# Kernel tuning notes

Measured on AMD Instinct MI355X. Metric: run time of the kernel, lower is better.

## Reference

```python
import jax, jax.numpy as jnp
import numpy as np

B, N, DIM, HEADS, RED = 8, 1024, 768, 12, 2
CR = DIM // RED  # 384 reduced channel dim
HD = CR // HEADS  # 32 head dim
EPS = 1e-5


def layer_norm(x, g, b):
    mu = jnp.mean(x, axis=-1, keepdims=True)
    var = jnp.var(x, axis=-1, keepdims=True)
    return (x - mu) * jax.lax.rsqrt(var + EPS) * g + b


def setup_inputs() -> dict:
    key = jax.random.key(0)
    ks = jax.random.split(key, 8)
    s_in = 1.0 / np.sqrt(DIM)
    s_cr = 1.0 / np.sqrt(CR)
    return {
        "x": jax.random.normal(ks[0], (B, N, DIM), dtype=jnp.float32),
        "ln0_g": jnp.ones((DIM,), jnp.float32),
        "ln0_b": jnp.zeros((DIM,), jnp.float32),
        "w_proj": jax.random.normal(ks[1], (CR, DIM), jnp.float32) * s_in,  # conv1x1 -> linear
        "b_proj": jnp.zeros((CR,), jnp.float32),
        "ln1_g": jnp.ones((CR,), jnp.float32),
        "ln1_b": jnp.zeros((CR,), jnp.float32),
        "wq": jax.random.normal(ks[2], (CR, CR), jnp.float32) * s_cr,
        "wk": jax.random.normal(ks[3], (CR, CR), jnp.float32) * s_cr,
        "wv": jax.random.normal(ks[4], (CR, CR), jnp.float32) * s_cr,
    }


def attention(y, wq, wk, wv):
    # y: [B, N, CR]; 1x1 conv == linear on channel dim
    def heads(w):
        return (y @ w.T).reshape(B, N, HEADS, HD).transpose(0, 2, 1, 3)  # [B,H,N,D]
    q, k, v = heads(wq), heads(wk), heads(wv)
    scale = HD ** -0.5
    attn = jax.nn.softmax(jnp.einsum("bhnd,bhmd->bhnm", q, k) * scale, axis=-1)
    out = jnp.einsum("bhnm,bhmd->bhnd", attn, v)  # [B,H,N,D]
    return out.transpose(0, 2, 1, 3).reshape(B, N, CR)


def reference(x, ln0_g, ln0_b, w_proj, b_proj, ln1_g, ln1_b, wq, wk, wv):
    h = layer_norm(x, ln0_g, ln0_b) @ w_proj.T + b_proj  # [B,N,CR]
    y = layer_norm(h, ln1_g, ln1_b)
    return h + attention(y, wq, wk, wv)
```

## Files before the change

### kernel.cpp

```cpp
#include <hip/hip_runtime.h>
#include <hip/hip_bf16.h>
#include <math.h>

#define BB 8
#define NN 1024
#define DIM 768
#define HEADS 12
#define CR 384
#define HD 32
#define MROWS (BB*NN)
#define EPS 1e-5f
#define SCALE_Q 0.25503486f

typedef __attribute__((ext_vector_type(8))) __bf16 bf16x8;
typedef __attribute__((ext_vector_type(8))) unsigned short u16x8;
typedef __attribute__((ext_vector_type(4))) float f32x4;

__device__ __forceinline__ unsigned short f2bf(float f) {
    unsigned int u = __float_as_uint(f);
    u += 0x7fffu + ((u >> 16) & 1u);
    return (unsigned short)(u >> 16);
}

__device__ __forceinline__ unsigned int packbf2(float lo, float hi) {
    __hip_bfloat162 h2 = __float22bfloat162_rn(make_float2(lo, hi));
    unsigned int u; __builtin_memcpy(&u, &h2, sizeof(u));
    return u;
}

__device__ __forceinline__ void async_cp16(const unsigned short* g, unsigned short* l) {
    __builtin_amdgcn_global_load_lds(
        (const __attribute__((address_space(1))) unsigned int*)g,
        (__attribute__((address_space(3))) unsigned int*)l, 16, 0, 0);
}

__global__ __launch_bounds__(256) void ln0_cast(
    const float* __restrict__ x,
    const float* __restrict__ g, const float* __restrict__ bt,
    unsigned short* __restrict__ a0,
    const float* __restrict__ wpf, const float* __restrict__ wq,
    const float* __restrict__ wk, const float* __restrict__ wv,
    unsigned short* __restrict__ wpo, unsigned short* __restrict__ wqkvo)
{
    const int bx = blockIdx.x;
    const int t = threadIdx.x;
    if (bx >= MROWS) {
        int i = (bx - MROWS) * 256 + t;
        const float* src; unsigned short* dst; int off;
        if (i < 73728) { src = wpf; dst = wpo; off = i; }
        else {
            int j = i - 73728;
            int sel = j / 36864; off = j % 36864;
            src = sel == 0 ? wq : (sel == 1 ? wk : wv);
            dst = wqkvo + (size_t)sel * 147456;
        }
        float4 v = ((const float4*)src)[off];
        ((ushort4*)dst)[off] = make_ushort4(f2bf(v.x), f2bf(v.y), f2bf(v.z), f2bf(v.w));
        return;
    }
    const int nv = DIM >> 2;
    const float* a = x + (size_t)bx * DIM;
    float4 val = make_float4(0.f, 0.f, 0.f, 0.f);
    float s = 0.f, ss = 0.f;
    if (t < nv) {
        val = ((const float4*)a)[t];
        s = val.x + val.y + val.z + val.w;
        ss = val.x * val.x + val.y * val.y + val.z * val.z + val.w * val.w;
    }
    for (int off = 32; off; off >>= 1) {
        s  += __shfl_down(s, off, 64);
        ss += __shfl_down(ss, off, 64);
    }
    __shared__ float rS[4], rSS[4];
    __shared__ float sh_mu, sh_rs;
    int lane = t & 63, w = t >> 6;
    if (lane == 0) { rS[w] = s; rSS[w] = ss; }
    __syncthreads();
    if (t == 0) {
        float S = rS[0] + rS[1] + rS[2] + rS[3];
        float SS = rSS[0] + rSS[1] + rSS[2] + rSS[3];
        float m = S / DIM;
        sh_mu = m;
        sh_rs = rsqrtf(SS / DIM - m * m + EPS);
    }
    __syncthreads();
    if (t < nv) {
        float m = sh_mu, r = sh_rs;
        float4 gv = ((const float4*)g)[t];
        float4 bv = ((const float4*)bt)[t];
        ((ushort4*)(a0 + (size_t)bx * DIM))[t] = make_ushort4(
            f2bf((val.x - m) * r * gv.x + bv.x),
            f2bf((val.y - m) * r * gv.y + bv.y),
            f2bf((val.z - m) * r * gv.z + bv.z),
            f2bf((val.w - m) * r * gv.w + bv.w));
    }
}

__global__ __launch_bounds__(128) void ln1_sum(
    const float* __restrict__ h0, const float* __restrict__ h1,
    const float* __restrict__ bias,
    const float* __restrict__ g, const float* __restrict__ bt,
    float* __restrict__ hs, unsigned short* __restrict__ y)
{
    const int row = blockIdx.x;
    const int t = threadIdx.x;
    const int nv = CR >> 2;
    float4 val = make_float4(0.f, 0.f, 0.f, 0.f);
    float s = 0.f, ss = 0.f;
    if (t < nv) {
        float4 v0 = ((const float4*)(h0 + (size_t)row * CR))[t];
        float4 v1 = ((const float4*)(h1 + (size_t)row * CR))[t];
        float4 bv = ((const float4*)bias)[t];
        val = make_float4(v0.x + v1.x + bv.x, v0.y + v1.y + bv.y,
                          v0.z + v1.z + bv.z, v0.w + v1.w + bv.w);
        ((float4*)(hs + (size_t)row * CR))[t] = val;
        s = val.x + val.y + val.z + val.w;
        ss = val.x * val.x + val.y * val.y + val.z * val.z + val.w * val.w;
    }
    for (int off = 32; off; off >>= 1) {
        s  += __shfl_down(s, off, 64);
        ss += __shfl_down(ss, off, 64);
    }
    __shared__ float rS[2], rSS[2];
    __shared__ float sh_mu, sh_rs;
    int lane = t & 63, w = t >> 6;
    if (lane == 0) { rS[w] = s; rSS[w] = ss; }
    __syncthreads();
    if (t == 0) {
        float S = rS[0] + rS[1];
        float SS = rSS[0] + rSS[1];
        float m = S / CR;
        sh_mu = m;
        sh_rs = rsqrtf(SS / CR - m * m + EPS);
    }
    __syncthreads();
    if (t < nv) {
        float m = sh_mu, r = sh_rs;
        float4 gv = ((const float4*)g)[t];
        float4 bv = ((const float4*)bt)[t];
        ((ushort4*)(y + (size_t)row * CR))[t] = make_ushort4(
            f2bf((val.x - m) * r * gv.x + bv.x),
            f2bf((val.y - m) * r * gv.y + bv.y),
            f2bf((val.z - m) * r * gv.z + bv.z),
            f2bf((val.w - m) * r * gv.w + bv.w));
    }
}

template<int KD, int NITER, int MODE>
__global__ __launch_bounds__(256) void gemm_mfma(
    const unsigned short* __restrict__ A,
    const unsigned short* __restrict__ W,
    void* __restrict__ C0, void* __restrict__ C1)
{
    __shared__ unsigned short Asm[2 * 128 * 32];
    __shared__ unsigned short Bsm[2 * 128 * 32];
    const int t = threadIdx.x;
    const int wave = t >> 6, lane = t & 63;
    const int l15 = lane & 15, quad = lane >> 4;
    const int m0 = blockIdx.y * 128;
    const int n0 = blockIdx.x * 128;
    const int koff = blockIdx.z * (NITER * 32);
    const int wm = (wave & 1) * 64, wn = (wave >> 1) * 64;

    const int srow = lane >> 2;
    const int skq  = (lane & 3) * 8;
    const unsigned short* gA = A + (size_t)(m0 + wave * 32 + srow) * KD + koff + skq;
    const unsigned short* gB = W + (size_t)(n0 + wave * 32 + srow) * KD + koff + skq;
    unsigned short* lA = Asm + wave * 1024;
    unsigned short* lB = Bsm + wave * 1024;

    async_cp16(gA, lA);
    async_cp16(gA + (size_t)16 * KD, lA + 512);
    async_cp16(gB, lB);
    async_cp16(gB + (size_t)16 * KD, lB + 512);

    f32x4 acc[4][4];
#pragma unroll
    for (int i = 0; i < 4; i++)
#pragma unroll
        for (int j = 0; j < 4; j++) acc[i][j] = (f32x4){0.f, 0.f, 0.f, 0.f};

    for (int it = 0; it < NITER; it++) {
        __syncthreads();
        const int cur = it & 1;
        if (it + 1 < NITER) {
            const int noff = (cur ^ 1) * 4096;
            async_cp16(gA + (it + 1) * 32, lA + noff);
            async_cp16(gA + (size_t)16 * KD + (it + 1) * 32, lA + noff + 512);
            async_cp16(gB + (it + 1) * 32, lB + noff);
            async_cp16(gB + (size_t)16 * KD + (it + 1) * 32, lB + noff + 512);
        }
        const unsigned short* Ab = Asm + cur * 4096;
        const unsigned short* Bb = Bsm + cur * 4096;
        bf16x8 af[4], bfr[4];
#pragma unroll
        for (int i = 0; i < 4; i++)
            af[i] = *(const bf16x8*)(Ab + (wm + i * 16 + l15) * 32 + quad * 8);
#pragma unroll
        for (int j = 0; j < 4; j++)
            bfr[j] = *(const bf16x8*)(Bb + (wn + j * 16 + l15) * 32 + quad * 8);
#pragma unroll
        for (int i = 0; i < 4; i++)
#pragma unroll
            for (int j = 0; j < 4; j++)
                acc[i][j] = __builtin_amdgcn_mfma_f32_16x16x32_bf16(af[i], bfr[j], acc[i][j], 0, 0, 0);
    }

    if constexpr (MODE == 0) {
        float* C = (float*)C0 + (size_t)blockIdx.z * MROWS * CR;
#pragma unroll
        for (int i = 0; i < 4; i++)
#pragma unroll
            for (int j = 0; j < 4; j++)
#pragma unroll
                for (int reg = 0; reg < 4; reg++) {
                    int row = m0 + wm + i * 16 + quad * 4 + reg;
                    int col = n0 + wn + j * 16 + l15;
                    C[(size_t)row * CR + col] = acc[i][j][reg];
                }
    } else {
        unsigned short* Cqk = (unsigned short*)C0;
        unsigned short* Vt  = (unsigned short*)C1;
#pragma unroll
        for (int i = 0; i < 4; i++)
#pragma unroll
            for (int j = 0; j < 4; j++) {
                const int colbase = n0 + wn + j * 16;
                const int token0 = m0 + wm + i * 16 + quad * 4;
                if (colbase < DIM) {
                    const float sc = (colbase < CR) ? SCALE_Q : 1.f;
#pragma unroll
                    for (int reg = 0; reg < 4; reg++)
                        Cqk[(size_t)(token0 + reg) * DIM + colbase + l15] = f2bf(acc[i][j][reg] * sc);
                } else {
                    const int ch = colbase - DIM + l15;
                    uint2 pk;
                    pk.x = packbf2(acc[i][j][0], acc[i][j][1]);
                    pk.y = packbf2(acc[i][j][2], acc[i][j][3]);
                    *(uint2*)(Vt + (size_t)ch * MROWS + token0) = pk;
                }
            }
    }
}

__global__ __launch_bounds__(256) void attn_mfma(
    const unsigned short* __restrict__ qk,
    const unsigned short* __restrict__ vt,
    const float* __restrict__ h, float* __restrict__ out)
{
    const int qt = blockIdx.x;
    const int bh = blockIdx.y;
    const int b = bh / HEADS, head = bh % HEADS;
    const int hc = head * HD;
    const int t = threadIdx.x;
    const int wave = t >> 6, lane = t & 63;
    const int l15 = lane & 15, quad = lane >> 4;
    const int q0 = qt * 128;

    __shared__ unsigned short Ks[2][64 * 40];
    __shared__ unsigned short Vs[2][32 * 72];
    __shared__ unsigned short Ps[4][32 * 72];
    unsigned short* Pw = Ps[wave];

    bf16x8 qa[2];
#pragma unroll
    for (int qi = 0; qi < 2; qi++)
        qa[qi] = *(const bf16x8*)(qk + (size_t)(b * NN + q0 + wave * 32 + qi * 16 + l15) * DIM
                                  + hc + quad * 8);

    const int rr = t >> 2, seg = t & 3;
    const unsigned short* gK = qk + (size_t)(b * NN + rr) * DIM + CR + hc + seg * 8;
    const int vch = wave * 8 + (lane >> 3), vko = (lane & 7) * 8;
    const unsigned short* gV = vt + (size_t)(hc + vch) * MROWS + b * NN + vko;

    {
        u16x8 k0 = *(const u16x8*)gK;
        u16x8 v0 = *(const u16x8*)gV;
        *(u16x8*)(Ks[0] + rr * 40 + seg * 8) = k0;
        *(u16x8*)(Vs[0] + vch * 72 + vko) = v0;
    }
    u16x8 kreg = *(const u16x8*)(gK + (size_t)64 * DIM);
    u16x8 vreg = *(const u16x8*)(gV + 64);

    f32x4 o[2][2] = {{{0.f,0.f,0.f,0.f},{0.f,0.f,0.f,0.f}},
                     {{0.f,0.f,0.f,0.f},{0.f,0.f,0.f,0.f}}};
    float lpart[2] = {0.f, 0.f};
    __syncthreads();

    for (int kt = 0; kt < 16; kt++) {
        const int cur = kt & 1;
        const unsigned short* Kc = Ks[cur];
        const unsigned short* Vc = Vs[cur];

        bf16x8 kb[4];
#pragma unroll
        for (int nt = 0; nt < 4; nt++)
            kb[nt] = *(const bf16x8*)(Kc + (nt * 16 + l15) * 40 + quad * 8);

#pragma unroll
        for (int qi = 0; qi < 2; qi++) {
            f32x4 s[4];
#pragma unroll
            for (int nt = 0; nt < 4; nt++) {
                f32x4 z = {0.f, 0.f, 0.f, 0.f};
                s[nt] = __builtin_amdgcn_mfma_f32_16x16x32_bf16(kb[nt], qa[qi], z, 0, 0, 0);
            }
#pragma unroll
            for (int nt = 0; nt < 4; nt++) {
                float e0 = __builtin_amdgcn_exp2f(s[nt][0]);
                float e1 = __builtin_amdgcn_exp2f(s[nt][1]);
                float e2 = __builtin_amdgcn_exp2f(s[nt][2]);
                float e3 = __builtin_amdgcn_exp2f(s[nt][3]);
                lpart[qi] += (e0 + e1) + (e2 + e3);
                uint2 pk;
                pk.x = packbf2(e0, e1);
                pk.y = packbf2(e2, e3);
                *(uint2*)(Pw + (qi * 16 + l15) * 72 + nt * 16 + quad * 4) = pk;
            }
        }

        bf16x8 vb[2][2];
#pragma unroll
        for (int kk = 0; kk < 2; kk++)
#pragma unroll
            for (int nt2 = 0; nt2 < 2; nt2++)
                vb[kk][nt2] = *(const bf16x8*)(Vc + (nt2 * 16 + l15) * 72 + kk * 32 + quad * 8);

#pragma unroll
        for (int qi = 0; qi < 2; qi++)
#pragma unroll
            for (int kk = 0; kk < 2; kk++) {
                bf16x8 pa = *(const bf16x8*)(Pw + (qi * 16 + l15) * 72 + kk * 32 + quad * 8);
#pragma unroll
                for (int nt2 = 0; nt2 < 2; nt2++)
                    o[qi][nt2] = __builtin_amdgcn_mfma_f32_16x16x32_bf16(pa, vb[kk][nt2], o[qi][nt2], 0, 0, 0);
            }

        if (kt < 15) {
            *(u16x8*)(Ks[cur ^ 1] + rr * 40 + seg * 8) = kreg;
            *(u16x8*)(Vs[cur ^ 1] + vch * 72 + vko) = vreg;
            if (kt < 14) {
                kreg = *(const u16x8*)(gK + (size_t)(kt + 2) * 64 * DIM);
                vreg = *(const u16x8*)(gV + (kt + 2) * 64);
            }
        }
        __syncthreads();
    }

#pragma unroll
    for (int qi = 0; qi < 2; qi++) {
        float l = lpart[qi];
        l += __shfl_xor(l, 16, 64);
        l += __shfl_xor(l, 32, 64);
        const float linv = 1.f / l;
#pragma unroll
        for (int reg = 0; reg < 4; reg++) {
            const float li = __shfl(linv, quad * 4 + reg, 64);
            const size_t row = (size_t)(b * NN + q0 + wave * 32 + qi * 16 + quad * 4 + reg);
#pragma unroll
            for (int nt2 = 0; nt2 < 2; nt2++) {
                size_t idx = row * CR + hc + nt2 * 16 + l15;
                out[idx] = h[idx] + o[qi][nt2][reg] * li;
            }
        }
    }
}

extern "C" void kernel_launch(void* const* d_in, const int* in_sizes, int n_in,
                              void* d_out, int out_size, void* d_ws, size_t ws_size,
                              hipStream_t stream) {
    const float* x      = (const float*)d_in[0];
    const float* ln0_g  = (const float*)d_in[1];
    const float* ln0_b  = (const float*)d_in[2];
    const float* w_proj = (const float*)d_in[3];
    const float* b_proj = (const float*)d_in[4];
    const float* ln1_g  = (const float*)d_in[5];
    const float* ln1_b  = (const float*)d_in[6];
    const float* wq     = (const float*)d_in[7];
    const float* wk     = (const float*)d_in[8];
    const float* wv     = (const float*)d_in[9];
    float* out = (float*)d_out;

    char* base = (char*)d_ws;
    unsigned short* a0   = (unsigned short*)base;
    unsigned short* qkb  = (unsigned short*)base;
    float*          hp   = (float*)(base + 12582912);
    float*          hbuf = (float*)(base + 37748736);
    unsigned short* yb   = (unsigned short*)(base + 50331648);
    unsigned short* vtb  = (unsigned short*)(base + 56623104);
    unsigned short* wp   = (unsigned short*)(base + 62914560);
    unsigned short* wqkv = (unsigned short*)(base + 63504384);

    ln0_cast<<<MROWS + 720, 256, 0, stream>>>(x, ln0_g, ln0_b, a0,
                                              w_proj, wq, wk, wv, wp, wqkv);
    gemm_mfma<DIM, 12, 0><<<dim3(CR / 128, MROWS / 128, 2), 256, 0, stream>>>(
        a0, wp, hp, nullptr);
    ln1_sum<<<MROWS, 128, 0, stream>>>(hp, hp + (size_t)MROWS * CR, b_proj,
                                       ln1_g, ln1_b, hbuf, yb);
    gemm_mfma<CR, 12, 1><<<dim3(1152 / 128, MROWS / 128, 1), 256, 0, stream>>>(
        yb, wqkv, qkb, vtb);
    attn_mfma<<<dim3(NN / 128, BB * HEADS), 256, 0, stream>>>(qkb, vtb, hbuf, out);
}
```

Baseline: 161.5 us.

## Store split-K projection partials as bf16 and use one wave per row in LN0

The two split-K partial outputs of the projection GEMM are now written as bf16 instead of fp32, and ln1_sum reads them as bf16 before summing, which halves that intermediate traffic. LN0 is restructured so each wave handles one row with xor-shuffle reductions, removing the shared-memory and __syncthreads reductions and cutting the block count from 8192 to 2048. Stores now use packed bf16 conversion, and workspace offsets are recompacted. Rounding the partials to bf16 before summing adds precision loss to the residual h.

```diff
diff --git a/kernel.cpp b/kernel.cpp
--- a/kernel.cpp
+++ b/kernel.cpp
@@ -26,6 +26,11 @@
     __hip_bfloat162 h2 = __float22bfloat162_rn(make_float2(lo, hi));
     unsigned int u; __builtin_memcpy(&u, &h2, sizeof(u));
     return u;
+}
+
+__device__ __forceinline__ float bf2f(unsigned short u) {
+    unsigned int w = ((unsigned int)u) << 16;
+    return __uint_as_float(w);
 }
 
 __device__ __forceinline__ void async_cp16(const unsigned short* g, unsigned short* l) {
@@ -44,8 +49,8 @@
 {
     const int bx = blockIdx.x;
     const int t = threadIdx.x;
-    if (bx >= MROWS) {
-        int i = (bx - MROWS) * 256 + t;
+    if (bx >= 2048) {
+        int i = (bx - 2048) * 256 + t;
         const float* src; unsigned short* dst; int off;
         if (i < 73728) { src = wpf; dst = wpo; off = i; }
         else {
@@ -55,49 +60,38 @@
             dst = wqkvo + (size_t)sel * 147456;
         }
         float4 v = ((const float4*)src)[off];
-        ((ushort4*)dst)[off] = make_ushort4(f2bf(v.x), f2bf(v.y), f2bf(v.z), f2bf(v.w));
+        uint2 pk; pk.x = packbf2(v.x, v.y); pk.y = packbf2(v.z, v.w);
+        ((uint2*)dst)[off] = pk;
         return;
     }
-    const int nv = DIM >> 2;
-    const float* a = x + (size_t)bx * DIM;
-    float4 val = make_float4(0.f, 0.f, 0.f, 0.f);
-    float s = 0.f, ss = 0.f;
-    if (t < nv) {
-        val = ((const float4*)a)[t];
-        s = val.x + val.y + val.z + val.w;
-        ss = val.x * val.x + val.y * val.y + val.z * val.z + val.w * val.w;
-    }
-    for (int off = 32; off; off >>= 1) {
-        s  += __shfl_down(s, off, 64);
-        ss += __shfl_down(ss, off, 64);
-    }
-    __shared__ float rS[4], rSS[4];
-    __shared__ float sh_mu, sh_rs;
-    int lane = t & 63, w = t >> 6;
-    if (lane == 0) { rS[w] = s; rSS[w] = ss; }
-    __syncthreads();
-    if (t == 0) {
-        float S = rS[0] + rS[1] + rS[2] + rS[3];
-        float SS = rSS[0] + rSS[1] + rSS[2] + rSS[3];
-        float m = S / DIM;
-        sh_mu = m;
-        sh_rs = rsqrtf(SS / DIM - m * m + EPS);
-    }
-    __syncthreads();
-    if (t < nv) {
-        float m = sh_mu, r = sh_rs;
-        float4 gv = ((const float4*)g)[t];
-        float4 bv = ((const float4*)bt)[t];
-        ((ushort4*)(a0 + (size_t)bx * DIM))[t] = make_ushort4(
-            f2bf((val.x - m) * r * gv.x + bv.x),
-            f2bf((val.y - m) * r * gv.y + bv.y),
-            f2bf((val.z - m) * r * gv.z + bv.z),
-            f2bf((val.w - m) * r * gv.w + bv.w));
+    const int wave = t >> 6, lane = t & 63;
+    const int row = bx * 4 + wave;
+    const float* a = x + (size_t)row * DIM;
+    float4 v[3]; float s = 0.f, ss = 0.f;
+#pragma unroll
+    for (int c = 0; c < 3; c++) {
+        v[c] = ((const float4*)a)[lane + c * 64];
+        s  += v[c].x + v[c].y + v[c].z + v[c].w;
+        ss += v[c].x * v[c].x + v[c].y * v[c].y + v[c].z * v[c].z + v[c].w * v[c].w;
+    }
+#pragma unroll
+    for (int off = 1; off < 64; off <<= 1) {
+        s += __shfl_xor(s, off, 64); ss += __shfl_xor(ss, off, 64);
+    }
+    const float mu = s / DIM, rs = rsqrtf(ss / DIM - mu * mu + EPS);
+#pragma unroll
+    for (int c = 0; c < 3; c++) {
+        float4 gv = ((const float4*)g)[lane + c * 64];
+        float4 bv = ((const float4*)bt)[lane + c * 64];
+        uint2 pk;
+        pk.x = packbf2((v[c].x - mu) * rs * gv.x + bv.x, (v[c].y - mu) * rs * gv.y + bv.y);
+        pk.y = packbf2((v[c].z - mu) * rs * gv.z + bv.z, (v[c].w - mu) * rs * gv.w + bv.w);
+        *(uint2*)(a0 + (size_t)row * DIM + (lane + c * 64) * 4) = pk;
     }
 }
 
 __global__ __launch_bounds__(128) void ln1_sum(
-    const float* __restrict__ h0, const float* __restrict__ h1,
+    const unsigned short* __restrict__ h0, const unsigned short* __restrict__ h1,
     const float* __restrict__ bias,
     const float* __restrict__ g, const float* __restrict__ bt,
     float* __restrict__ hs, unsigned short* __restrict__ y)
@@ -108,11 +102,13 @@
     float4 val = make_float4(0.f, 0.f, 0.f, 0.f);
     float s = 0.f, ss = 0.f;
     if (t < nv) {
-        float4 v0 = ((const float4*)(h0 + (size_t)row * CR))[t];
-        float4 v1 = ((const float4*)(h1 + (size_t)row * CR))[t];
+        ushort4 p0 = ((const ushort4*)(h0 + (size_t)row * CR))[t];
+        ushort4 p1 = ((const ushort4*)(h1 + (size_t)row * CR))[t];
         float4 bv = ((const float4*)bias)[t];
-        val = make_float4(v0.x + v1.x + bv.x, v0.y + v1.y + bv.y,
-                          v0.z + v1.z + bv.z, v0.w + v1.w + bv.w);
+        val = make_float4(bf2f(p0.x) + bf2f(p1.x) + bv.x,
+                          bf2f(p0.y) + bf2f(p1.y) + bv.y,
+                          bf2f(p0.z) + bf2f(p1.z) + bv.z,
+                          bf2f(p0.w) + bf2f(p1.w) + bv.w);
         ((float4*)(hs + (size_t)row * CR))[t] = val;
         s = val.x + val.y + val.z + val.w;
         ss = val.x * val.x + val.y * val.y + val.z * val.z + val.w * val.w;
@@ -138,11 +134,10 @@
         float m = sh_mu, r = sh_rs;
         float4 gv = ((const float4*)g)[t];
         float4 bv = ((const float4*)bt)[t];
-        ((ushort4*)(y + (size_t)row * CR))[t] = make_ushort4(
-            f2bf((val.x - m) * r * gv.x + bv.x),
-            f2bf((val.y - m) * r * gv.y + bv.y),
-            f2bf((val.z - m) * r * gv.z + bv.z),
-            f2bf((val.w - m) * r * gv.w + bv.w));
+        uint2 pk;
+        pk.x = packbf2((val.x - m) * r * gv.x + bv.x, (val.y - m) * r * gv.y + bv.y);
+        pk.y = packbf2((val.z - m) * r * gv.z + bv.z, (val.w - m) * r * gv.w + bv.w);
+        *(uint2*)(y + (size_t)row * CR + t * 4) = pk;
     }
 }
 
@@ -207,7 +202,7 @@
     }
 
     if constexpr (MODE == 0) {
-        float* C = (float*)C0 + (size_t)blockIdx.z * MROWS * CR;
+        unsigned short* C = (unsigned short*)C0 + (size_t)blockIdx.z * MROWS * CR;
 #pragma unroll
         for (int i = 0; i < 4; i++)
 #pragma unroll
@@ -216,7 +211,7 @@
                 for (int reg = 0; reg < 4; reg++) {
                     int row = m0 + wm + i * 16 + quad * 4 + reg;
                     int col = n0 + wn + j * 16 + l15;
-                    C[(size_t)row * CR + col] = acc[i][j][reg];
+                    C[(size_t)row * CR + col] = f2bf(acc[i][j][reg]);
                 }
     } else {
         unsigned short* Cqk = (unsigned short*)C0;
@@ -384,15 +379,15 @@
     char* base = (char*)d_ws;
     unsigned short* a0   = (unsigned short*)base;
     unsigned short* qkb  = (unsigned short*)base;
-    float*          hp   = (float*)(base + 12582912);
-    float*          hbuf = (float*)(base + 37748736);
-    unsigned short* yb   = (unsigned short*)(base + 50331648);
-    unsigned short* vtb  = (unsigned short*)(base + 56623104);
-    unsigned short* wp   = (unsigned short*)(base + 62914560);
-    unsigned short* wqkv = (unsigned short*)(base + 63504384);
-
-    ln0_cast<<<MROWS + 720, 256, 0, stream>>>(x, ln0_g, ln0_b, a0,
-                                              w_proj, wq, wk, wv, wp, wqkv);
+    unsigned short* hp   = (unsigned short*)(base + 12582912);
+    float*          hbuf = (float*)(base + 25165824);
+    unsigned short* yb   = (unsigned short*)(base + 37748736);
+    unsigned short* vtb  = (unsigned short*)(base + 44040192);
+    unsigned short* wp   = (unsigned short*)(base + 50331648);
+    unsigned short* wqkv = (unsigned short*)(base + 50921472);
+
+    ln0_cast<<<2048 + 720, 256, 0, stream>>>(x, ln0_g, ln0_b, a0,
+                                             w_proj, wq, wk, wv, wp, wqkv);
     gemm_mfma<DIM, 12, 0><<<dim3(CR / 128, MROWS / 128, 2), 256, 0, stream>>>(
         a0, wp, hp, nullptr);
     ln1_sum<<<MROWS, 128, 0, stream>>>(hp, hp + (size_t)MROWS * CR, b_proj,
```

Measured after the change: 158.7 us. Within noise of the previous version (-1.7%).
